# Kernel tuning notes

Hardware: AMD Instinct MI355X
Metric: run time of the kernel (lower is better)

Reference implementation:

```python
import jax, jax.numpy as jnp
import numpy as np

H = 16
D_MODEL = 1024
D_K = D_MODEL // H  # 64


def setup_inputs() -> dict:
    key = jax.random.key(0)
    ks = jax.random.split(key, 8)
    B, S = 8, 1024
    q = jax.random.normal(ks[0], (B, S, D_MODEL), dtype=jnp.float32)
    k = jax.random.normal(ks[1], (B, S, D_MODEL), dtype=jnp.float32)
    v = jax.random.normal(ks[2], (B, S, D_MODEL), dtype=jnp.float32)
    # xavier_normal for [h, d_model, d_k]: std = sqrt(2 / (d_model + d_k)) (fan over last two dims)
    std_p = float(np.sqrt(2.0 / (D_MODEL + D_K)))
    W_q = jax.random.normal(ks[3], (H, D_MODEL, D_K), dtype=jnp.float32) * std_p
    W_k = jax.random.normal(ks[4], (H, D_MODEL, D_K), dtype=jnp.float32) * std_p
    W_v = jax.random.normal(ks[5], (H, D_MODEL, D_K), dtype=jnp.float32) * std_p
    std_o = float(np.sqrt(2.0 / (H * D_K + D_MODEL)))
    W_o = jax.random.normal(ks[6], (D_MODEL, H * D_K), dtype=jnp.float32) * std_o  # torch Linear weight [out, in]
    b_o = jax.random.normal(ks[7], (D_MODEL,), dtype=jnp.float32) * 0.01
    return {"q": q, "k": k, "v": v, "W_q": W_q, "W_k": W_k, "W_v": W_v, "W_o": W_o, "b_o": b_o}


def reference(q, k, v, W_q, W_k, W_v, W_o, b_o):
    B, S, _ = q.shape
    # per-head projections: [h, b, s, d_k]
    qh = jnp.einsum('bsd,hdk->hbsk', q, W_q)
    kh = jnp.einsum('bsd,hdk->hbsk', k, W_k)
    vh = jnp.einsum('bsd,hdk->hbsk', v, W_v)
    scale = 1.0 / jnp.sqrt(jnp.asarray(D_K, dtype=q.dtype))
    scores = jnp.einsum('hbsk,hbtk->hbst', qh, kh) * scale  # [h,b,s,s]
    attn = jax.nn.softmax(scores, axis=-1)
    c = jnp.einsum('hbst,hbtk->hbsk', attn, vh)  # [h,b,s,d_k]
    # torch code splits the stacked (h*b) batch and concats on feature dim:
    # head index becomes the OUTER factor of the feature dim -> [b,s,h*d_k]
    c = jnp.transpose(c, (1, 2, 0, 3)).reshape(B, S, H * D_K)
    out = c @ W_o.T + b_o
    return out
```

## Files before the change

kernel.cpp:

```cpp
#include <hip/hip_runtime.h>
#include <hip/hip_bf16.h>

typedef __bf16 bf16_t;
typedef __attribute__((ext_vector_type(8))) __bf16 bf16x8;
typedef __attribute__((ext_vector_type(4))) float f32x4;

#define MFMA(a, b, c) __builtin_amdgcn_mfma_f32_16x16x32_bf16(a, b, c, 0, 0, 0)

__global__ void fill_sentinel(float* out, int n, float val) {
  int i = blockIdx.x * blockDim.x + threadIdx.x;
  if (i < n) out[i] = val;
}

__global__ void transpose_w(const float* __restrict__ Wq, const float* __restrict__ Wk,
                            const float* __restrict__ Wv, bf16_t* __restrict__ Wt) {
  int gid = blockIdx.x * blockDim.x + threadIdx.x;
  int e = gid * 8;
  int m = e >> 20;
  int rem = e & 1048575;
  int n = rem >> 10;
  int d0 = rem & 1023;
  const float* W = (m == 0) ? Wq : (m == 1) ? Wk : Wv;
  int h = n >> 6, kk = n & 63;
  union { bf16_t h8[8]; uint4 u; } tmp;
#pragma unroll
  for (int j = 0; j < 8; ++j)
    tmp.h8[j] = (bf16_t)W[((size_t)(h * 1024 + d0 + j)) * 64 + kk];
  *(uint4*)(Wt + e) = tmp.u;
}

__device__ inline bf16x8 ld8(const bf16_t* p) { return *(const bf16x8*)p; }
__device__ inline bf16x8 ld8(const float* p) {
  f32x4 a = *(const f32x4*)p;
  f32x4 b = *(const f32x4*)(p + 4);
  bf16x8 r;
  r[0] = (bf16_t)a[0]; r[1] = (bf16_t)a[1]; r[2] = (bf16_t)a[2]; r[3] = (bf16_t)a[3];
  r[4] = (bf16_t)b[0]; r[5] = (bf16_t)b[1]; r[6] = (bf16_t)b[2]; r[7] = (bf16_t)b[3];
  return r;
}

template <int MODE, typename TA>
__global__ void gemm_bt(const TA* __restrict__ A, const void* __restrict__ Bt_,
                        const float* __restrict__ bias, void* __restrict__ out_,
                        int M, int N, int K) {
  constexpr int PAD = 40;
  __shared__ bf16_t sA[128 * PAD];
  __shared__ bf16_t sB[128 * PAD];
  const int t = threadIdx.x;
  const int w = t >> 6, l = t & 63;
  const int lq = l >> 4, ll = l & 15;
  const int m0 = blockIdx.x * 128, n0 = blockIdx.y * 128;
  const int wr = (w >> 1) * 64, wc = (w & 1) * 64;
  f32x4 acc[4][4] = {};
  for (int k0 = 0; k0 < K; k0 += 32) {
    __syncthreads();
#pragma unroll
    for (int r = 0; r < 2; ++r) {
      int e = (r * 256 + t) * 8;
      int row = e >> 5, col = e & 31;
      *(bf16x8*)(sA + row * PAD + col) = ld8(A + (size_t)(m0 + row) * K + k0 + col);
      if (MODE == 2)
        *(bf16x8*)(sB + row * PAD + col) =
            ld8((const float*)Bt_ + (size_t)(n0 + row) * K + k0 + col);
      else
        *(bf16x8*)(sB + row * PAD + col) =
            ld8((const bf16_t*)Bt_ + (size_t)(n0 + row) * K + k0 + col);
    }
    __syncthreads();
    bf16x8 af[4], bfr[4];
#pragma unroll
    for (int i = 0; i < 4; ++i) {
      af[i]  = *(const bf16x8*)(sA + (wr + i * 16 + ll) * PAD + lq * 8);
      bfr[i] = *(const bf16x8*)(sB + (wc + i * 16 + ll) * PAD + lq * 8);
    }
#pragma unroll
    for (int mi = 0; mi < 4; ++mi)
#pragma unroll
      for (int ni = 0; ni < 4; ++ni)
        acc[mi][ni] = MFMA(af[mi], bfr[ni], acc[mi][ni]);
  }
#pragma unroll
  for (int mi = 0; mi < 4; ++mi)
#pragma unroll
    for (int ni = 0; ni < 4; ++ni)
#pragma unroll
      for (int r = 0; r < 4; ++r) {
        int row = m0 + wr + mi * 16 + lq * 4 + r;
        int col = n0 + wc + ni * 16 + ll;
        float v = acc[mi][ni][r];
        if (MODE == 2) {
          ((float*)out_)[(size_t)row * N + col] = v + bias[col];
        } else {
          int h = col >> 6, kk = col & 63, b = row >> 10, s = row & 1023;
          size_t idx;
          if (MODE == 0)
            idx = ((size_t)((h * 8 + b) * 1024 + s)) * 64 + kk;
          else
            idx = ((size_t)((h * 8 + b) * 64 + kk)) * 1024 + s;
          ((bf16_t*)out_)[idx] = (bf16_t)v;
        }
      }
}

__global__ void attn_kernel(const bf16_t* __restrict__ qh, const bf16_t* __restrict__ kh,
                            const bf16_t* __restrict__ vt, bf16_t* __restrict__ c) {
  constexpr int QP = 72, KP = 72, VP = 136, PP = 136;
  __shared__ bf16_t sQ[64 * QP];
  __shared__ bf16_t sK[128 * KP];
  __shared__ bf16_t sV[64 * VP];
  __shared__ bf16_t sP[4][16 * PP];
  const int t = threadIdx.x;
  const int w = t >> 6, l = t & 63;
  const int lq = l >> 4, ll = l & 15;
  const int q0 = blockIdx.x * 64;
  const int hb = blockIdx.y;
  const int h = hb >> 3, b = hb & 7;
  const size_t base = (size_t)hb * 65536;
  const bf16_t* Q = qh + base + (size_t)q0 * 64;
  const bf16_t* K = kh + base;
  const bf16_t* V = vt + base;
#pragma unroll
  for (int r = 0; r < 2; ++r) {
    int e = (r * 256 + t) * 8;
    int row = e >> 6, col = e & 63;
    *(uint4*)(sQ + row * QP + col) = *(const uint4*)(Q + e);
  }
  float mrow[4], lrow[4];
  f32x4 o[4] = {};
#pragma unroll
  for (int r = 0; r < 4; ++r) { mrow[r] = -1e30f; lrow[r] = 0.f; }

  for (int kt = 0; kt < 1024; kt += 128) {
    __syncthreads();
#pragma unroll
    for (int r = 0; r < 4; ++r) {
      int e = (r * 256 + t) * 8;
      int row = e >> 6, col = e & 63;
      *(uint4*)(sK + row * KP + col) = *(const uint4*)(K + (size_t)kt * 64 + e);
      int rowv = e >> 7, colv = e & 127;
      *(uint4*)(sV + rowv * VP + colv) =
          *(const uint4*)(V + (size_t)rowv * 1024 + kt + colv);
    }
    __syncthreads();
    f32x4 sacc[8] = {};
    bf16x8 aq[2];
#pragma unroll
    for (int ks = 0; ks < 2; ++ks)
      aq[ks] = *(const bf16x8*)(sQ + (w * 16 + ll) * QP + ks * 32 + lq * 8);
#pragma unroll
    for (int ni = 0; ni < 8; ++ni)
#pragma unroll
      for (int ks = 0; ks < 2; ++ks) {
        bf16x8 bk = *(const bf16x8*)(sK + (ni * 16 + ll) * KP + ks * 32 + lq * 8);
        sacc[ni] = MFMA(aq[ks], bk, sacc[ni]);
      }
    float rmax[4] = {-1e30f, -1e30f, -1e30f, -1e30f};
#pragma unroll
    for (int ni = 0; ni < 8; ++ni)
#pragma unroll
      for (int r = 0; r < 4; ++r) {
        sacc[ni][r] *= 0.125f;
        rmax[r] = fmaxf(rmax[r], sacc[ni][r]);
      }
#pragma unroll
    for (int off = 1; off < 16; off <<= 1)
#pragma unroll
      for (int r = 0; r < 4; ++r)
        rmax[r] = fmaxf(rmax[r], __shfl_xor(rmax[r], off));
    float alpha[4];
#pragma unroll
    for (int r = 0; r < 4; ++r) {
      float mnew = fmaxf(mrow[r], rmax[r]);
      alpha[r] = __expf(mrow[r] - mnew);
      mrow[r] = mnew;
    }
    float rs[4] = {0.f, 0.f, 0.f, 0.f};
#pragma unroll
    for (int ni = 0; ni < 8; ++ni)
#pragma unroll
      for (int r = 0; r < 4; ++r) {
        float p = __expf(sacc[ni][r] - mrow[r]);
        sacc[ni][r] = p;
        rs[r] += p;
      }
#pragma unroll
    for (int off = 1; off < 16; off <<= 1)
#pragma unroll
      for (int r = 0; r < 4; ++r)
        rs[r] += __shfl_xor(rs[r], off);
#pragma unroll
    for (int r = 0; r < 4; ++r)
      lrow[r] = lrow[r] * alpha[r] + rs[r];
#pragma unroll
    for (int ni = 0; ni < 4; ++ni)
#pragma unroll
      for (int r = 0; r < 4; ++r)
        o[ni][r] *= alpha[r];
    bf16_t* Pw = sP[w];
#pragma unroll
    for (int ni = 0; ni < 8; ++ni)
#pragma unroll
      for (int r = 0; r < 4; ++r)
        Pw[(lq * 4 + r) * PP + ni * 16 + ll] = (bf16_t)sacc[ni][r];
    asm volatile("s_waitcnt lgkmcnt(0)" ::: "memory");
#pragma unroll
    for (int ks = 0; ks < 4; ++ks) {
      bf16x8 ap = *(const bf16x8*)(Pw + ll * PP + ks * 32 + lq * 8);
#pragma unroll
      for (int ni = 0; ni < 4; ++ni) {
        bf16x8 bv = *(const bf16x8*)(sV + (ni * 16 + ll) * VP + ks * 32 + lq * 8);
        o[ni] = MFMA(ap, bv, o[ni]);
      }
    }
  }
#pragma unroll
  for (int ni = 0; ni < 4; ++ni)
#pragma unroll
    for (int r = 0; r < 4; ++r) {
      int s = q0 + w * 16 + lq * 4 + r;
      int dk = ni * 16 + ll;
      float val = o[ni][r] / lrow[r];
      c[((size_t)(b * 1024 + s)) * 1024 + h * 64 + dk] = (bf16_t)val;
    }
}

extern "C" void kernel_launch(void* const* d_in, const int* in_sizes, int n_in,
                              void* d_out, int out_size, void* d_ws, size_t ws_size,
                              hipStream_t stream) {
  float* out = (float*)d_out;
  int nblk_out = (out_size + 255) / 256;
  if (n_in != 8) {
    fill_sentinel<<<nblk_out, 256, 0, stream>>>(out, out_size, 600.0f + 10.0f * n_in);
    return;
  }
  const int expect[8] = {8388608, 8388608, 8388608, 1048576,
                         1048576, 1048576, 1048576, 1024};
  for (int i = 0; i < 8; ++i)
    if (in_sizes[i] != expect[i]) {
      fill_sentinel<<<nblk_out, 256, 0, stream>>>(out, out_size, 500.0f + 10.0f * i);
      return;
    }

  bf16_t* ws   = (bf16_t*)d_ws;
  bf16_t* qhb  = ws;
  bf16_t* khb  = ws + 8388608;
  bf16_t* vtb  = ws + 16777216;
  bf16_t* Wt   = ws + 25165824;
  bf16_t* cbuf = ws + 25165824;
  if (ws_size < 67108864ull) {
    fill_sentinel<<<nblk_out, 256, 0, stream>>>(out, out_size, 400.0f);
    return;
  }

  const float* q  = (const float*)d_in[0];
  const float* k  = (const float*)d_in[1];
  const float* v  = (const float*)d_in[2];
  const float* Wq = (const float*)d_in[3];
  const float* Wk = (const float*)d_in[4];
  const float* Wv = (const float*)d_in[5];
  const float* Wo = (const float*)d_in[6];
  const float* bo = (const float*)d_in[7];

  transpose_w<<<1536, 256, 0, stream>>>(Wq, Wk, Wv, Wt);
  dim3 gg(64, 8);
  gemm_bt<0, float><<<gg, 256, 0, stream>>>(q, Wt,           nullptr, qhb, 8192, 1024, 1024);
  gemm_bt<0, float><<<gg, 256, 0, stream>>>(k, Wt + 1048576, nullptr, khb, 8192, 1024, 1024);
  gemm_bt<1, float><<<gg, 256, 0, stream>>>(v, Wt + 2097152, nullptr, vtb, 8192, 1024, 1024);
  attn_kernel<<<dim3(16, 128), 256, 0, stream>>>(qhb, khb, vtb, cbuf);
  gemm_bt<2, bf16_t><<<gg, 256, 0, stream>>>(cbuf, Wo, bo, out, 8192, 1024, 1024);
}
```

Before: 473.0 us.

## Restage GEMM tiles via direct LDS loads and drop LDS staging in attention

The GEMMs now stage fp32 operands in LDS as fp32 and convert to bf16 at fragment-read time, and load bf16 operands with global_load_lds straight into unpadded LDS. The attention kernel drops its shared K/V tiles and block barriers, reading K and V fragments directly from global memory per wave with a swapped grid order so blocks of one head run together. The softmax scale and log2(e) are folded into the Q projection so exp2f replaces __expf. The aim is to cut barrier and LDS staging overhead, but each wave now fetches K/V from global/L2 separately, and the unpadded bf16 LDS layout may cause bank conflicts.

Result: slower. 592.5 us (+25.3%).

```diff
diff --git a/kernel.cpp b/kernel.cpp
--- a/kernel.cpp
+++ b/kernel.cpp
@@ -6,6 +6,19 @@
 typedef __attribute__((ext_vector_type(4))) float f32x4;
 
 #define MFMA(a, b, c) __builtin_amdgcn_mfma_f32_16x16x32_bf16(a, b, c, 0, 0, 0)
+
+typedef __attribute__((address_space(3))) unsigned int as3_u32;
+typedef const __attribute__((address_space(1))) unsigned int as1_u32;
+__device__ inline void gl_lds16(const void* g, void* lds) {
+  __builtin_amdgcn_global_load_lds((as1_u32*)g, (as3_u32*)lds, 16, 0, 0);
+}
+
+__device__ inline bf16x8 cvt_bf8(f32x4 a, f32x4 b) {
+  bf16x8 r;
+  r[0] = (bf16_t)a[0]; r[1] = (bf16_t)a[1]; r[2] = (bf16_t)a[2]; r[3] = (bf16_t)a[3];
+  r[4] = (bf16_t)b[0]; r[5] = (bf16_t)b[1]; r[6] = (bf16_t)b[2]; r[7] = (bf16_t)b[3];
+  return r;
+}
 
 __global__ void fill_sentinel(float* out, int n, float val) {
   int i = blockIdx.x * blockDim.x + threadIdx.x;
@@ -29,23 +42,15 @@
   *(uint4*)(Wt + e) = tmp.u;
 }
 
-__device__ inline bf16x8 ld8(const bf16_t* p) { return *(const bf16x8*)p; }
-__device__ inline bf16x8 ld8(const float* p) {
-  f32x4 a = *(const f32x4*)p;
-  f32x4 b = *(const f32x4*)(p + 4);
-  bf16x8 r;
-  r[0] = (bf16_t)a[0]; r[1] = (bf16_t)a[1]; r[2] = (bf16_t)a[2]; r[3] = (bf16_t)a[3];
-  r[4] = (bf16_t)b[0]; r[5] = (bf16_t)b[1]; r[6] = (bf16_t)b[2]; r[7] = (bf16_t)b[3];
-  return r;
-}
-
-template <int MODE, typename TA>
-__global__ void gemm_bt(const TA* __restrict__ A, const void* __restrict__ Bt_,
-                        const float* __restrict__ bias, void* __restrict__ out_,
-                        int M, int N, int K) {
-  constexpr int PAD = 40;
-  __shared__ bf16_t sA[128 * PAD];
-  __shared__ bf16_t sB[128 * PAD];
+template <int MODE, bool AF32, bool BF32>
+__global__ __launch_bounds__(256) void gemm2(const void* __restrict__ A_,
+                                             const void* __restrict__ B_,
+                                             const float* __restrict__ bias,
+                                             void* __restrict__ out_,
+                                             int M, int N, int K, float scale) {
+  constexpr int FP = 36;
+  __shared__ __align__(16) char sAraw[AF32 ? 128 * FP * 4 : 128 * 32 * 2];
+  __shared__ __align__(16) char sBraw[BF32 ? 128 * FP * 4 : 128 * 32 * 2];
   const int t = threadIdx.x;
   const int w = t >> 6, l = t & 63;
   const int lq = l >> 4, ll = l & 15;
@@ -54,24 +59,58 @@
   f32x4 acc[4][4] = {};
   for (int k0 = 0; k0 < K; k0 += 32) {
     __syncthreads();
-#pragma unroll
-    for (int r = 0; r < 2; ++r) {
-      int e = (r * 256 + t) * 8;
-      int row = e >> 5, col = e & 31;
-      *(bf16x8*)(sA + row * PAD + col) = ld8(A + (size_t)(m0 + row) * K + k0 + col);
-      if (MODE == 2)
-        *(bf16x8*)(sB + row * PAD + col) =
-            ld8((const float*)Bt_ + (size_t)(n0 + row) * K + k0 + col);
-      else
-        *(bf16x8*)(sB + row * PAD + col) =
-            ld8((const bf16_t*)Bt_ + (size_t)(n0 + row) * K + k0 + col);
+    if constexpr (AF32) {
+      const float* A = (const float*)A_;
+      float* sA = (float*)sAraw;
+#pragma unroll
+      for (int r = 0; r < 4; ++r) {
+        int e = (r * 256 + t) * 4, row = e >> 5, col = e & 31;
+        *(f32x4*)(sA + row * FP + col) =
+            *(const f32x4*)(A + (size_t)(m0 + row) * K + k0 + col);
+      }
+    } else {
+      const bf16_t* A = (const bf16_t*)A_;
+#pragma unroll
+      for (int r = 0; r < 2; ++r) {
+        int e = (r * 256 + t) * 8, row = e >> 5, col = e & 31;
+        gl_lds16(A + (size_t)(m0 + row) * K + k0 + col, sAraw + e * 2);
+      }
+    }
+    if constexpr (BF32) {
+      const float* B = (const float*)B_;
+      float* sB = (float*)sBraw;
+#pragma unroll
+      for (int r = 0; r < 4; ++r) {
+        int e = (r * 256 + t) * 4, row = e >> 5, col = e & 31;
+        *(f32x4*)(sB + row * FP + col) =
+            *(const f32x4*)(B + (size_t)(n0 + row) * K + k0 + col);
+      }
+    } else {
+      const bf16_t* B = (const bf16_t*)B_;
+#pragma unroll
+      for (int r = 0; r < 2; ++r) {
+        int e = (r * 256 + t) * 8, row = e >> 5, col = e & 31;
+        gl_lds16(B + (size_t)(n0 + row) * K + k0 + col, sBraw + e * 2);
+      }
     }
     __syncthreads();
     bf16x8 af[4], bfr[4];
 #pragma unroll
     for (int i = 0; i < 4; ++i) {
-      af[i]  = *(const bf16x8*)(sA + (wr + i * 16 + ll) * PAD + lq * 8);
-      bfr[i] = *(const bf16x8*)(sB + (wc + i * 16 + ll) * PAD + lq * 8);
+      if constexpr (AF32) {
+        const float* sA = (const float*)sAraw;
+        int ro = (wr + i * 16 + ll) * FP + lq * 8;
+        af[i] = cvt_bf8(*(const f32x4*)(sA + ro), *(const f32x4*)(sA + ro + 4));
+      } else {
+        af[i] = *(const bf16x8*)((const bf16_t*)sAraw + (wr + i * 16 + ll) * 32 + lq * 8);
+      }
+      if constexpr (BF32) {
+        const float* sB = (const float*)sBraw;
+        int ro = (wc + i * 16 + ll) * FP + lq * 8;
+        bfr[i] = cvt_bf8(*(const f32x4*)(sB + ro), *(const f32x4*)(sB + ro + 4));
+      } else {
+        bfr[i] = *(const bf16x8*)((const bf16_t*)sBraw + (wc + i * 16 + ll) * 32 + lq * 8);
+      }
     }
 #pragma unroll
     for (int mi = 0; mi < 4; ++mi)
@@ -87,7 +126,7 @@
       for (int r = 0; r < 4; ++r) {
         int row = m0 + wr + mi * 16 + lq * 4 + r;
         int col = n0 + wc + ni * 16 + ll;
-        float v = acc[mi][ni][r];
+        float v = acc[mi][ni][r] * scale;
         if (MODE == 2) {
           ((float*)out_)[(size_t)row * N + col] = v + bias[col];
         } else {
@@ -102,76 +141,55 @@
       }
 }
 
-__global__ void attn_kernel(const bf16_t* __restrict__ qh, const bf16_t* __restrict__ kh,
-                            const bf16_t* __restrict__ vt, bf16_t* __restrict__ c) {
-  constexpr int QP = 72, KP = 72, VP = 136, PP = 136;
-  __shared__ bf16_t sQ[64 * QP];
-  __shared__ bf16_t sK[128 * KP];
-  __shared__ bf16_t sV[64 * VP];
+__global__ __launch_bounds__(256) void attn3(const bf16_t* __restrict__ qh,
+                                             const bf16_t* __restrict__ kh,
+                                             const bf16_t* __restrict__ vt,
+                                             bf16_t* __restrict__ c) {
+  constexpr int PP = 132;
   __shared__ bf16_t sP[4][16 * PP];
   const int t = threadIdx.x;
   const int w = t >> 6, l = t & 63;
   const int lq = l >> 4, ll = l & 15;
-  const int q0 = blockIdx.x * 64;
-  const int hb = blockIdx.y;
-  const int h = hb >> 3, b = hb & 7;
+  const int hb = blockIdx.x, h = hb >> 3, b = hb & 7;
+  const int q0 = blockIdx.y * 64 + w * 16;
   const size_t base = (size_t)hb * 65536;
-  const bf16_t* Q = qh + base + (size_t)q0 * 64;
+  const bf16_t* Q = qh + base;
   const bf16_t* K = kh + base;
   const bf16_t* V = vt + base;
-#pragma unroll
-  for (int r = 0; r < 2; ++r) {
-    int e = (r * 256 + t) * 8;
-    int row = e >> 6, col = e & 63;
-    *(uint4*)(sQ + row * QP + col) = *(const uint4*)(Q + e);
-  }
+  bf16_t* Pw = sP[w];
+  bf16x8 aq[2];
+#pragma unroll
+  for (int ks = 0; ks < 2; ++ks)
+    aq[ks] = *(const bf16x8*)(Q + (size_t)(q0 + ll) * 64 + ks * 32 + lq * 8);
   float mrow[4], lrow[4];
   f32x4 o[4] = {};
 #pragma unroll
   for (int r = 0; r < 4; ++r) { mrow[r] = -1e30f; lrow[r] = 0.f; }
 
   for (int kt = 0; kt < 1024; kt += 128) {
-    __syncthreads();
-#pragma unroll
-    for (int r = 0; r < 4; ++r) {
-      int e = (r * 256 + t) * 8;
-      int row = e >> 6, col = e & 63;
-      *(uint4*)(sK + row * KP + col) = *(const uint4*)(K + (size_t)kt * 64 + e);
-      int rowv = e >> 7, colv = e & 127;
-      *(uint4*)(sV + rowv * VP + colv) =
-          *(const uint4*)(V + (size_t)rowv * 1024 + kt + colv);
-    }
-    __syncthreads();
     f32x4 sacc[8] = {};
-    bf16x8 aq[2];
-#pragma unroll
-    for (int ks = 0; ks < 2; ++ks)
-      aq[ks] = *(const bf16x8*)(sQ + (w * 16 + ll) * QP + ks * 32 + lq * 8);
+#pragma unroll
+    for (int ni = 0; ni < 8; ++ni) {
+      const bf16_t* kp = K + (size_t)(kt + ni * 16 + ll) * 64 + lq * 8;
+      bf16x8 b0 = *(const bf16x8*)kp;
+      bf16x8 b1 = *(const bf16x8*)(kp + 32);
+      sacc[ni] = MFMA(aq[0], b0, sacc[ni]);
+      sacc[ni] = MFMA(aq[1], b1, sacc[ni]);
+    }
+    float rmax[4] = {-1e30f, -1e30f, -1e30f, -1e30f};
 #pragma unroll
     for (int ni = 0; ni < 8; ++ni)
 #pragma unroll
-      for (int ks = 0; ks < 2; ++ks) {
-        bf16x8 bk = *(const bf16x8*)(sK + (ni * 16 + ll) * KP + ks * 32 + lq * 8);
-        sacc[ni] = MFMA(aq[ks], bk, sacc[ni]);
-      }
-    float rmax[4] = {-1e30f, -1e30f, -1e30f, -1e30f};
-#pragma unroll
-    for (int ni = 0; ni < 8; ++ni)
-#pragma unroll
-      for (int r = 0; r < 4; ++r) {
-        sacc[ni][r] *= 0.125f;
-        rmax[r] = fmaxf(rmax[r], sacc[ni][r]);
-      }
+      for (int r = 0; r < 4; ++r) rmax[r] = fmaxf(rmax[r], sacc[ni][r]);
 #pragma unroll
     for (int off = 1; off < 16; off <<= 1)
 #pragma unroll
-      for (int r = 0; r < 4; ++r)
-        rmax[r] = fmaxf(rmax[r], __shfl_xor(rmax[r], off));
+      for (int r = 0; r < 4; ++r) rmax[r] = fmaxf(rmax[r], __shfl_xor(rmax[r], off));
     float alpha[4];
 #pragma unroll
     for (int r = 0; r < 4; ++r) {
       float mnew = fmaxf(mrow[r], rmax[r]);
-      alpha[r] = __expf(mrow[r] - mnew);
+      alpha[r] = exp2f(mrow[r] - mnew);
       mrow[r] = mnew;
     }
     float rs[4] = {0.f, 0.f, 0.f, 0.f};
@@ -179,24 +197,20 @@
     for (int ni = 0; ni < 8; ++ni)
 #pragma unroll
       for (int r = 0; r < 4; ++r) {
-        float p = __expf(sacc[ni][r] - mrow[r]);
+        float p = exp2f(sacc[ni][r] - mrow[r]);
         sacc[ni][r] = p;
         rs[r] += p;
       }
 #pragma unroll
     for (int off = 1; off < 16; off <<= 1)
 #pragma unroll
-      for (int r = 0; r < 4; ++r)
-        rs[r] += __shfl_xor(rs[r], off);
-#pragma unroll
-    for (int r = 0; r < 4; ++r)
-      lrow[r] = lrow[r] * alpha[r] + rs[r];
+      for (int r = 0; r < 4; ++r) rs[r] += __shfl_xor(rs[r], off);
+#pragma unroll
+    for (int r = 0; r < 4; ++r) lrow[r] = lrow[r] * alpha[r] + rs[r];
 #pragma unroll
     for (int ni = 0; ni < 4; ++ni)
 #pragma unroll
-      for (int r = 0; r < 4; ++r)
-        o[ni][r] *= alpha[r];
-    bf16_t* Pw = sP[w];
+      for (int r = 0; r < 4; ++r) o[ni][r] *= alpha[r];
 #pragma unroll
     for (int ni = 0; ni < 8; ++ni)
 #pragma unroll
@@ -208,7 +222,7 @@
       bf16x8 ap = *(const bf16x8*)(Pw + ll * PP + ks * 32 + lq * 8);
 #pragma unroll
       for (int ni = 0; ni < 4; ++ni) {
-        bf16x8 bv = *(const bf16x8*)(sV + (ni * 16 + ll) * VP + ks * 32 + lq * 8);
+        bf16x8 bv = *(const bf16x8*)(V + (size_t)(ni * 16 + ll) * 1024 + kt + ks * 32 + lq * 8);
         o[ni] = MFMA(ap, bv, o[ni]);
       }
     }
@@ -217,10 +231,9 @@
   for (int ni = 0; ni < 4; ++ni)
 #pragma unroll
     for (int r = 0; r < 4; ++r) {
-      int s = q0 + w * 16 + lq * 4 + r;
+      int s = q0 + lq * 4 + r;
       int dk = ni * 16 + ll;
-      float val = o[ni][r] / lrow[r];
-      c[((size_t)(b * 1024 + s)) * 1024 + h * 64 + dk] = (bf16_t)val;
+      c[((size_t)(b * 1024 + s)) * 1024 + h * 64 + dk] = (bf16_t)(o[ni][r] / lrow[r]);
     }
 }
 
@@ -240,7 +253,6 @@
       fill_sentinel<<<nblk_out, 256, 0, stream>>>(out, out_size, 500.0f + 10.0f * i);
       return;
     }
-
   bf16_t* ws   = (bf16_t*)d_ws;
   bf16_t* qhb  = ws;
   bf16_t* khb  = ws + 8388608;
@@ -261,11 +273,13 @@
   const float* Wo = (const float*)d_in[6];
   const float* bo = (const float*)d_in[7];
 
+  const float QSCALE = 0.18033688011112043f;
+
   transpose_w<<<1536, 256, 0, stream>>>(Wq, Wk, Wv, Wt);
   dim3 gg(64, 8);
-  gemm_bt<0, float><<<gg, 256, 0, stream>>>(q, Wt,           nullptr, qhb, 8192, 1024, 1024);
-  gemm_bt<0, float><<<gg, 256, 0, stream>>>(k, Wt + 1048576, nullptr, khb, 8192, 1024, 1024);
-  gemm_bt<1, float><<<gg, 256, 0, stream>>>(v, Wt + 2097152, nullptr, vtb, 8192, 1024, 1024);
-  attn_kernel<<<dim3(16, 128), 256, 0, stream>>>(qhb, khb, vtb, cbuf);
-  gemm_bt<2, bf16_t><<<gg, 256, 0, stream>>>(cbuf, Wo, bo, out, 8192, 1024, 1024);
-}
+  gemm2<0, true, false><<<gg, 256, 0, stream>>>(q, Wt,           nullptr, qhb, 8192, 1024, 1024, QSCALE);
+  gemm2<0, true, false><<<gg, 256, 0, stream>>>(k, Wt + 1048576, nullptr, khb, 8192, 1024, 1024, 1.0f);
+  gemm2<1, true, false><<<gg, 256, 0, stream>>>(v, Wt + 2097152, nullptr, vtb, 8192, 1024, 1024, 1.0f);
+  attn3<<<dim3(128, 16), 256, 0, stream>>>(qhb, khb, vtb, cbuf);
+  gemm2<2, false, true><<<gg, 256, 0, stream>>>(cbuf, Wo, bo, out, 8192, 1024, 1024, 1.0f);
+}
```
